# Kernel optimization log

Hardware: AMD Instinct MI355X
Metric: run time of the kernel (lower is better)

The kernel has to match this reference:

```python
import jax, jax.numpy as jnp
import numpy as np

B, T, D = 4, 1024, 1024
H, S = 16, 64            # n_heads, stalk_dim
HID = 3072               # int(D*3.0), already even
P_ADIC_BASE, P_ADIC_MAX = 2, 16


def quant6(w):
    # per-tensor symmetric 6-bit fake-quant (abs-max scale, round, clamp)
    scale = jnp.abs(w).max() / 31.0 + 1e-8
    return jnp.clip(jnp.round(w / scale), -31, 31) * scale


def q6_ste(w):
    # straight-through estimator: identity gradient
    return w + jax.lax.stop_gradient(quant6(w) - w)


def layernorm(x, g, b, eps=1e-5):
    mu = x.mean(-1, keepdims=True)
    var = ((x - mu) ** 2).mean(-1, keepdims=True)
    return (x - mu) * jax.lax.rsqrt(var + eps) * g + b


def build_p_adic_bias(t, p=P_ADIC_BASE, max_val=P_ADIC_MAX):
    idx = np.arange(t)
    d = np.abs(idx[:, None] - idx[None, :])
    nz = d > 0
    vp = np.zeros_like(d)
    work = d.copy()
    while True:
        div = nz & (work % p == 0)
        if not div.any():
            break
        vp = vp + div.astype(vp.dtype)
        work = np.where(div, work // p, work)
    vals = np.minimum(vp, max_val).astype(np.float32)
    vals = np.where(nz, vals, np.float32(max_val))
    return jnp.asarray(vals / max_val)


def setup_inputs() -> dict:
    key = jax.random.key(0)
    ks = jax.random.split(key, 12)
    sd_d = 1.0 / np.sqrt(D)
    sd_s = 1.0 / np.sqrt(S)
    sd_h = 1.0 / np.sqrt(HID)
    return {
        "x": jax.random.normal(ks[0], (B, T, D), jnp.float32),
        "wq": jax.random.normal(ks[1], (D, D), jnp.float32) * sd_d,
        "wk": jax.random.normal(ks[2], (D, D), jnp.float32) * sd_d,
        "wv": jax.random.normal(ks[3], (D, D), jnp.float32) * sd_d,
        "wo": jax.random.normal(ks[4], (D, D), jnp.float32) * sd_d,
        "su": jax.random.normal(ks[5], (S, S), jnp.float32) * sd_s,
        "sv": jax.random.normal(ks[6], (S, S), jnp.float32) * sd_s,
        "p_scale": jnp.ones((1,), jnp.float32) * 0.1,
        "norm1_g": jnp.ones((D,), jnp.float32),
        "norm1_b": jnp.zeros((D,), jnp.float32),
        "norm2_g": jnp.ones((D,), jnp.float32),
        "norm2_b": jnp.zeros((D,), jnp.float32),
        "w_up": jax.random.normal(ks[7], (HID, D), jnp.float32) * sd_d,
        "w_down": jax.random.normal(ks[8], (D, HID), jnp.float32) * sd_h,
        "theta": jnp.zeros((HID // 2,), jnp.float32),
        "mlp_norm_g": jnp.ones((HID,), jnp.float32),
        "mlp_norm_b": jnp.zeros((HID,), jnp.float32),
    }


def _sheaf_attention(xn, wq, wk, wv, wo, su, sv, p_scale):
    # projections with inline 6-bit fake-quant of weights
    Q = (xn @ q6_ste(wq).T).reshape(B, T, H, S).transpose(0, 2, 1, 3)  # [B,H,T,S]
    K = (xn @ q6_ste(wk).T).reshape(B, T, H, S).transpose(0, 2, 1, 3)
    V = (xn @ q6_ste(wv).T).reshape(B, T, H, S).transpose(0, 2, 1, 3)
    Qs = Q @ q6_ste(su).T   # stalk map on head dim
    Ks = K @ q6_ste(sv).T
    scale = 1.0 / np.sqrt(S)
    scores = jnp.einsum('bhts,bhus->bhtu', Qs, Ks) * scale
    p_bias = build_p_adic_bias(T)                     # [T,T], constant
    scores = scores + p_scale[0] * p_bias[None, None]
    causal = jnp.triu(jnp.ones((T, T), bool), k=1)
    scores = jnp.where(causal[None, None], -jnp.inf, scores)
    attn = jax.nn.softmax(scores, axis=-1)
    out = jnp.einsum('bhtu,bhus->bhts', attn, V)
    out = out.transpose(0, 2, 1, 3).reshape(B, T, D)
    return out @ q6_ste(wo).T


def _so2_mlp(xn, w_up, w_down, theta, ng, nb):
    h = xn @ q6_ste(w_up).T                          # [B,T,HID]
    hp = h.reshape(B, T, HID // 2, 2)
    a, b = hp[..., 0], hp[..., 1]
    c, s = jnp.cos(theta), jnp.sin(theta)            # [HID/2]
    rot = jnp.stack([c * a - s * b, s * a + c * b], axis=-1).reshape(B, T, HID)
    rot = layernorm(rot, ng, nb)
    rot = jax.nn.silu(rot)
    return rot @ q6_ste(w_down).T


def reference(x, wq, wk, wv, wo, su, sv, p_scale, norm1_g, norm1_b,
              norm2_g, norm2_b, w_up, w_down, theta, mlp_norm_g, mlp_norm_b):
    # pre-norm residual block: x = x + attn(ln1(x)); x = x + mlp(ln2(x))
    x = x + _sheaf_attention(layernorm(x, norm1_g, norm1_b),
                             wq, wk, wv, wo, su, sv, p_scale)
    x = x + _so2_mlp(layernorm(x, norm2_g, norm2_b),
                     w_up, w_down, theta, mlp_norm_g, mlp_norm_b)
    return x
```

## Files before the change

kernel.cpp:

```cpp
#include <hip/hip_runtime.h>
#include <stdint.h>

typedef __bf16 bf16;
typedef __attribute__((ext_vector_type(8))) __bf16 bf16x8;
typedef __attribute__((ext_vector_type(4))) __bf16 bf16x4;
typedef __attribute__((ext_vector_type(2))) __bf16 bf16x2;
typedef __attribute__((ext_vector_type(4))) float f32x4;

#define GLOBAL_AS __attribute__((address_space(1)))
#define LDS_AS __attribute__((address_space(3)))

static __device__ __forceinline__ bf16 f2bf(float f) {
  unsigned u = __builtin_bit_cast(unsigned, f);
  u += 0x7fffu + ((u >> 16) & 1u);
  unsigned short h = (unsigned short)(u >> 16);
  return __builtin_bit_cast(bf16, h);
}

static __device__ __forceinline__ float waveSum(float v) {
  #pragma unroll
  for (int o = 32; o > 0; o >>= 1) v += __shfl_xor(v, o);
  return v;
}
static __device__ __forceinline__ float waveMax(float v) {
  #pragma unroll
  for (int o = 32; o > 0; o >>= 1) v = fmaxf(v, __shfl_xor(v, o));
  return v;
}

struct QTask { const float* src; bf16* dst; int n; int slot; int blk0; };
struct QTasks { QTask t[8]; };

__global__ __launch_bounds__(256) void absmax_all(QTasks qt, unsigned* amax) {
  int ti = 0;
  #pragma unroll
  for (int i = 1; i < 8; ++i) if ((int)blockIdx.x >= qt.t[i].blk0) ti = i;
  const QTask tk = qt.t[ti];
  const int base = (blockIdx.x - tk.blk0) * 4096;
  const float4* s4 = (const float4*)(tk.src + base);
  float m = 0.f;
  #pragma unroll
  for (int i = 0; i < 4; ++i) {
    float4 w = s4[i * 256 + threadIdx.x];
    m = fmaxf(m, fmaxf(fmaxf(fabsf(w.x), fabsf(w.y)), fmaxf(fabsf(w.z), fabsf(w.w))));
  }
  m = waveMax(m);
  __shared__ float red[4];
  if ((threadIdx.x & 63) == 0) red[threadIdx.x >> 6] = m;
  __syncthreads();
  if (threadIdx.x == 0) {
    float mm = fmaxf(fmaxf(red[0], red[1]), fmaxf(red[2], red[3]));
    atomicMax(amax + tk.slot, __float_as_uint(mm));
  }
}

__global__ __launch_bounds__(256) void quant_all(QTasks qt, const unsigned* amax) {
  int ti = 0;
  #pragma unroll
  for (int i = 1; i < 8; ++i) if ((int)blockIdx.x >= qt.t[i].blk0) ti = i;
  const QTask tk = qt.t[ti];
  const float scale = __uint_as_float(amax[tk.slot]) / 31.0f + 1e-8f;
  const int base = (blockIdx.x - tk.blk0) * 4096;
  const float4* s4 = (const float4*)(tk.src + base);
  bf16x4* d4 = (bf16x4*)(tk.dst + base);
  #pragma unroll
  for (int i = 0; i < 4; ++i) {
    float4 w = s4[i * 256 + threadIdx.x];
    bf16x4 o;
    float q;
    q = fminf(31.f, fmaxf(-31.f, rintf(w.x / scale))); o[0] = f2bf(q * scale);
    q = fminf(31.f, fmaxf(-31.f, rintf(w.y / scale))); o[1] = f2bf(q * scale);
    q = fminf(31.f, fmaxf(-31.f, rintf(w.z / scale))); o[2] = f2bf(q * scale);
    q = fminf(31.f, fmaxf(-31.f, rintf(w.w / scale))); o[3] = f2bf(q * scale);
    d4[i * 256 + threadIdx.x] = o;
  }
}

__global__ __launch_bounds__(256) void ln_kernel(const float* __restrict__ x,
                                                 const float* __restrict__ g,
                                                 const float* __restrict__ b,
                                                 bf16* __restrict__ out) {
  const int row = blockIdx.x, tid = threadIdx.x;
  const float4 v = ((const float4*)(x + (size_t)row * 1024))[tid];
  float s = v.x + v.y + v.z + v.w;
  float ss = v.x * v.x + v.y * v.y + v.z * v.z + v.w * v.w;
  s = waveSum(s); ss = waveSum(ss);
  __shared__ float rs[4], rq[4];
  if ((tid & 63) == 0) { rs[tid >> 6] = s; rq[tid >> 6] = ss; }
  __syncthreads();
  s = rs[0] + rs[1] + rs[2] + rs[3];
  ss = rq[0] + rq[1] + rq[2] + rq[3];
  const float mu = s * (1.f / 1024.f);
  const float var = ss * (1.f / 1024.f) - mu * mu;
  const float rstd = rsqrtf(var + 1e-5f);
  const float4 gv = ((const float4*)g)[tid];
  const float4 bv = ((const float4*)b)[tid];
  bf16x4 o;
  o[0] = f2bf((v.x - mu) * rstd * gv.x + bv.x);
  o[1] = f2bf((v.y - mu) * rstd * gv.y + bv.y);
  o[2] = f2bf((v.z - mu) * rstd * gv.z + bv.z);
  o[3] = f2bf((v.w - mu) * rstd * gv.w + bv.w);
  ((bf16x4*)(out + (size_t)row * 1024))[tid] = o;
}

template <int OUTMODE>
__global__ __launch_bounds__(256) void gemm_bt(const bf16* __restrict__ A,
                                               const bf16* __restrict__ B,
                                               void* __restrict__ C,
                                               const float* __restrict__ Res,
                                               int M, int N, int K) {
  constexpr int BM = 128, BN = 128, BK = 32;
  __shared__ bf16 As[BM * BK];
  __shared__ bf16 Bs[BN * BK];
  const int tid = threadIdx.x;
  const int wave = tid >> 6, lane = tid & 63, quad = lane >> 4, l16 = lane & 15;
  const int bm0 = blockIdx.y * BM, bn0 = blockIdx.x * BN;
  const int wr = (wave >> 1) * 64, wc = (wave & 1) * 64;
  f32x4 acc[4][4] = {};

  for (int k0 = 0; k0 < K; k0 += BK) {
    __syncthreads();
    #pragma unroll
    for (int i = 0; i < 2; ++i) {
      const int id = tid + i * 256;
      const int r = id >> 2, c = (id & 3) * 8;
      __builtin_amdgcn_global_load_lds(
          (GLOBAL_AS void*)(A + (size_t)(bm0 + r) * K + k0 + c),
          (LDS_AS void*)(As + (size_t)(i * 256 + wave * 64) * 8), 16, 0, 0);
      __builtin_amdgcn_global_load_lds(
          (GLOBAL_AS void*)(B + (size_t)(bn0 + r) * K + k0 + c),
          (LDS_AS void*)(Bs + (size_t)(i * 256 + wave * 64) * 8), 16, 0, 0);
    }
    __syncthreads();
    bf16x8 af[4], bfr[4];
    #pragma unroll
    for (int mi = 0; mi < 4; ++mi)
      af[mi] = *(const bf16x8*)(As + (wr + mi * 16 + l16) * BK + quad * 8);
    #pragma unroll
    for (int ni = 0; ni < 4; ++ni)
      bfr[ni] = *(const bf16x8*)(Bs + (wc + ni * 16 + l16) * BK + quad * 8);
    #pragma unroll
    for (int mi = 0; mi < 4; ++mi)
      #pragma unroll
      for (int ni = 0; ni < 4; ++ni)
        acc[mi][ni] = __builtin_amdgcn_mfma_f32_16x16x32_bf16(af[mi], bfr[ni], acc[mi][ni], 0, 0, 0);
  }

  #pragma unroll
  for (int mi = 0; mi < 4; ++mi)
    #pragma unroll
    for (int ni = 0; ni < 4; ++ni)
      #pragma unroll
      for (int reg = 0; reg < 4; ++reg) {
        const int row = bm0 + wr + mi * 16 + quad * 4 + reg;
        const int col = bn0 + wc + ni * 16 + l16;
        const size_t idx = (size_t)row * N + col;
        const float v = acc[mi][ni][reg];
        if constexpr (OUTMODE == 0) ((bf16*)C)[idx] = f2bf(v);
        else if constexpr (OUTMODE == 1) ((float*)C)[idx] = v;
        else ((float*)C)[idx] = Res[idx] + v;
      }
}

__global__ __launch_bounds__(256) void stalk_kernel(const bf16* __restrict__ QKV,
                                                    const bf16* __restrict__ Su,
                                                    const bf16* __restrict__ Sv,
                                                    bf16* __restrict__ Qsout,
                                                    bf16* __restrict__ Ksout) {
  constexpr int LDP = 72;
  const int sel = blockIdx.y;
  const bf16* W = sel ? Sv : Su;
  const bf16* src = QKV + (sel ? 1024 : 0);
  bf16* out = sel ? Ksout : Qsout;
  const int vbase = blockIdx.x * 128;
  const int tid = threadIdx.x, wave = tid >> 6, lane = tid & 63, quad = lane >> 4, l16 = lane & 15;
  __shared__ bf16 Ws[64 * LDP];
  #pragma unroll
  for (int i = 0; i < 2; ++i) {
    const int cid = tid + i * 256;
    const int n = cid >> 3, c8 = (cid & 7) * 8;
    *(bf16x8*)(Ws + n * LDP + c8) = *(const bf16x8*)(W + n * 64 + c8);
  }
  __syncthreads();
  f32x4 acc[2][4] = {};
  #pragma unroll
  for (int mi = 0; mi < 2; ++mi) {
    const int v = vbase + wave * 32 + mi * 16 + l16;
    const bf16* arow = src + (size_t)(v >> 4) * 3072 + (v & 15) * 64;
    const bf16x8 a0 = *(const bf16x8*)(arow + quad * 8);
    const bf16x8 a1 = *(const bf16x8*)(arow + 32 + quad * 8);
    #pragma unroll
    for (int ni = 0; ni < 4; ++ni) {
      const bf16x8 b0 = *(const bf16x8*)(Ws + (ni * 16 + l16) * LDP + quad * 8);
      const bf16x8 b1 = *(const bf16x8*)(Ws + (ni * 16 + l16) * LDP + 32 + quad * 8);
      acc[mi][ni] = __builtin_amdgcn_mfma_f32_16x16x32_bf16(a0, b0, acc[mi][ni], 0, 0, 0);
      acc[mi][ni] = __builtin_amdgcn_mfma_f32_16x16x32_bf16(a1, b1, acc[mi][ni], 0, 0, 0);
    }
  }
  #pragma unroll
  for (int mi = 0; mi < 2; ++mi)
    #pragma unroll
    for (int ni = 0; ni < 4; ++ni)
      #pragma unroll
      for (int reg = 0; reg < 4; ++reg) {
        const int v = vbase + wave * 32 + mi * 16 + quad * 4 + reg;
        const int b = v >> 14, t = (v >> 4) & 1023, h = v & 15;
        out[(((size_t)(b * 16 + h)) * 1024 + t) * 64 + ni * 16 + l16] = f2bf(acc[mi][ni][reg]);
      }
}

__global__ __launch_bounds__(256) void v_transpose(const bf16* __restrict__ QKV,
                                                   bf16* __restrict__ Vt) {
  constexpr int LDP = 72;
  const int bh = blockIdx.x, b = bh >> 4, h = bh & 15;
  const int t0 = blockIdx.y * 64;
  const int tid = threadIdx.x;
  __shared__ bf16 tile[64 * LDP];
  #pragma unroll
  for (int i = 0; i < 2; ++i) {
    const int cid = tid + i * 256;
    const int t = cid >> 3, c8 = (cid & 7) * 8;
    *(bf16x8*)(tile + t * LDP + c8) =
        *(const bf16x8*)(QKV + ((size_t)(b * 1024 + t0 + t)) * 3072 + 2048 + h * 64 + c8);
  }
  __syncthreads();
  #pragma unroll
  for (int i = 0; i < 2; ++i) {
    const int cid = tid + i * 256;
    const int s = cid >> 3, t8 = (cid & 7) * 8;
    bf16x8 o;
    #pragma unroll
    for (int j = 0; j < 8; ++j) o[j] = tile[(t8 + j) * LDP + s];
    *(bf16x8*)(Vt + ((size_t)(bh * 64 + s)) * 1024 + t0 + t8) = o;
  }
}

__global__ __launch_bounds__(256) void attn_flash(const bf16* __restrict__ Qs,
                                                  const bf16* __restrict__ Ks,
                                                  const bf16* __restrict__ Vtg,
                                                  const float* __restrict__ p_scale_ptr,
                                                  bf16* __restrict__ out) {
  constexpr int LDP = 72;
  const int bh = blockIdx.x;
  const int b = bh >> 4, h = bh & 15;
  const int ttile = 15 - (int)blockIdx.y;
  const int t0 = ttile * 64;
  const int tid = threadIdx.x, wave = tid >> 6, lane = tid & 63, quad = lane >> 4, l16 = lane & 15;

  __shared__ bf16 Kst[64 * LDP];
  __shared__ bf16 Vt[64 * LDP];
  __shared__ bf16 Plds[4][16 * LDP];

  const float pscale2 = p_scale_ptr[0] * 1.44269504f;
  const float sc2 = 0.125f * 1.44269504f;

  const bf16* Qb = Qs + ((size_t)bh * 1024 + t0) * 64;
  const bf16* Kb = Ks + ((size_t)bh * 1024) * 64;
  const bf16* Vb = Vtg + ((size_t)bh * 64) * 1024;

  const int trow = wave * 16 + l16;
  const bf16x8 qf0 = *(const bf16x8*)(Qb + trow * 64 + quad * 8);
  const bf16x8 qf1 = *(const bf16x8*)(Qb + trow * 64 + 32 + quad * 8);

  float m[4], lsum[4];
  f32x4 Oacc[4] = {};
  #pragma unroll
  for (int r = 0; r < 4; ++r) { m[r] = -1e30f; lsum[r] = 0.f; }

  bf16x8 st[4];
  auto loadTile = [&](int u0) {
    #pragma unroll
    for (int i = 0; i < 2; ++i) {
      const int cid = tid + i * 256;
      st[i] = *(const bf16x8*)(Kb + (size_t)u0 * 64 + cid * 8);
      st[2 + i] = *(const bf16x8*)(Vb + (size_t)(cid >> 3) * 1024 + u0 + (cid & 7) * 8);
    }
  };
  loadTile(0);

  for (int ut = 0; ut <= ttile; ++ut) {
    const int u0 = ut * 64;
    #pragma unroll
    for (int i = 0; i < 2; ++i) {
      const int cid = tid + i * 256;
      const int r = cid >> 3, c8 = (cid & 7) * 8;
      *(bf16x8*)(Kst + r * LDP + c8) = st[i];
      *(bf16x8*)(Vt + r * LDP + c8) = st[2 + i];
    }
    __syncthreads();
    if (ut < ttile) loadTile(u0 + 64);

    f32x4 sc[4];
    #pragma unroll
    for (int ni = 0; ni < 4; ++ni) {
      const bf16x8 k0 = *(const bf16x8*)(Kst + (ni * 16 + l16) * LDP + quad * 8);
      const bf16x8 k1 = *(const bf16x8*)(Kst + (ni * 16 + l16) * LDP + 32 + quad * 8);
      f32x4 z = {};
      z = __builtin_amdgcn_mfma_f32_16x16x32_bf16(qf0, k0, z, 0, 0, 0);
      z = __builtin_amdgcn_mfma_f32_16x16x32_bf16(qf1, k1, z, 0, 0, 0);
      sc[ni] = z;
    }
    const bool diag = (ut == ttile);
    float pv[4][4];
    #pragma unroll
    for (int reg = 0; reg < 4; ++reg) {
      const int t = t0 + wave * 16 + quad * 4 + reg;
      float mx = -1e30f;
      #pragma unroll
      for (int ni = 0; ni < 4; ++ni) {
        const int u = u0 + ni * 16 + l16;
        const int d = t - u;
        float v = sc[ni][reg] * sc2;
        if (diag && d < 0) {
          v = -1e30f;
        } else {
          const float bias = (d == 0) ? 1.0f : (float)__builtin_ctz(d) * 0.0625f;
          v += pscale2 * bias;
        }
        pv[reg][ni] = v;
        mx = fmaxf(mx, v);
      }
      #pragma unroll
      for (int o = 1; o < 16; o <<= 1) mx = fmaxf(mx, __shfl_xor(mx, o));
      const float mnew = fmaxf(m[reg], mx);
      const float alpha = exp2f(m[reg] - mnew);
      m[reg] = mnew;
      float rs = 0.f;
      #pragma unroll
      for (int ni = 0; ni < 4; ++ni) {
        const float p = exp2f(pv[reg][ni] - mnew);
        pv[reg][ni] = p;
        rs += p;
      }
      #pragma unroll
      for (int o = 1; o < 16; o <<= 1) rs += __shfl_xor(rs, o);
      lsum[reg] = lsum[reg] * alpha + rs;
      #pragma unroll
      for (int ni = 0; ni < 4; ++ni) Oacc[ni][reg] *= alpha;
    }
    #pragma unroll
    for (int reg = 0; reg < 4; ++reg)
      #pragma unroll
      for (int ni = 0; ni < 4; ++ni)
        Plds[wave][(quad * 4 + reg) * LDP + ni * 16 + l16] = f2bf(pv[reg][ni]);
    const bf16x8 pf0 = *(const bf16x8*)(&Plds[wave][l16 * LDP + quad * 8]);
    const bf16x8 pf1 = *(const bf16x8*)(&Plds[wave][l16 * LDP + 32 + quad * 8]);
    #pragma unroll
    for (int ni = 0; ni < 4; ++ni) {
      const bf16x8 v0 = *(const bf16x8*)(Vt + (ni * 16 + l16) * LDP + quad * 8);
      const bf16x8 v1 = *(const bf16x8*)(Vt + (ni * 16 + l16) * LDP + 32 + quad * 8);
      Oacc[ni] = __builtin_amdgcn_mfma_f32_16x16x32_bf16(pf0, v0, Oacc[ni], 0, 0, 0);
      Oacc[ni] = __builtin_amdgcn_mfma_f32_16x16x32_bf16(pf1, v1, Oacc[ni], 0, 0, 0);
    }
    __syncthreads();
  }

  #pragma unroll
  for (int ni = 0; ni < 4; ++ni)
    #pragma unroll
    for (int reg = 0; reg < 4; ++reg) {
      const int t = t0 + wave * 16 + quad * 4 + reg;
      out[((size_t)(b * 1024 + t)) * 1024 + h * 64 + ni * 16 + l16] = f2bf(Oacc[ni][reg] / lsum[reg]);
    }
}

__global__ __launch_bounds__(256) void rot_ln_silu(const bf16* __restrict__ hb,
                                                   const float* __restrict__ theta,
                                                   const float* __restrict__ g,
                                                   const float* __restrict__ bb,
                                                   bf16* __restrict__ out) {
  const int row = blockIdx.x, tid = threadIdx.x;
  const bf16* hr = hb + (size_t)row * 3072;
  float r[12];
  float s = 0.f, ss = 0.f;
  #pragma unroll
  for (int i = 0; i < 6; ++i) {
    const int p = tid + i * 256;
    const bf16x2 ab = *(const bf16x2*)(hr + 2 * p);
    const float a = (float)ab[0], b_ = (float)ab[1];
    const float th = theta[p];
    const float c = cosf(th), sn = sinf(th);
    const float r0 = c * a - sn * b_;
    const float r1 = sn * a + c * b_;
    r[2 * i] = r0; r[2 * i + 1] = r1;
    s += r0 + r1;
    ss += r0 * r0 + r1 * r1;
  }
  s = waveSum(s); ss = waveSum(ss);
  __shared__ float rs_[4], rq_[4];
  if ((tid & 63) == 0) { rs_[tid >> 6] = s; rq_[tid >> 6] = ss; }
  __syncthreads();
  s = rs_[0] + rs_[1] + rs_[2] + rs_[3];
  ss = rq_[0] + rq_[1] + rq_[2] + rq_[3];
  const float mu = s * (1.f / 3072.f);
  const float var = ss * (1.f / 3072.f) - mu * mu;
  const float rstd = rsqrtf(var + 1e-5f);
  bf16* orow = out + (size_t)row * 3072;
  #pragma unroll
  for (int i = 0; i < 6; ++i) {
    const int p = tid + i * 256;
    const float2 gv = *(const float2*)(g + 2 * p);
    const float2 bv = *(const float2*)(bb + 2 * p);
    const float y0 = (r[2 * i] - mu) * rstd * gv.x + bv.x;
    const float y1 = (r[2 * i + 1] - mu) * rstd * gv.y + bv.y;
    const float o0 = y0 / (1.f + expf(-y0));
    const float o1 = y1 / (1.f + expf(-y1));
    bf16x2 o; o[0] = f2bf(o0); o[1] = f2bf(o1);
    *(bf16x2*)(orow + 2 * p) = o;
  }
}

extern "C" void kernel_launch(void* const* d_in, const int* in_sizes, int n_in,
                              void* d_out, int out_size, void* d_ws, size_t ws_size,
                              hipStream_t stream) {
  const float* x    = (const float*)d_in[0];
  const float* wq   = (const float*)d_in[1];
  const float* wk   = (const float*)d_in[2];
  const float* wv   = (const float*)d_in[3];
  const float* wo   = (const float*)d_in[4];
  const float* su   = (const float*)d_in[5];
  const float* sv   = (const float*)d_in[6];
  const float* psc  = (const float*)d_in[7];
  const float* n1g  = (const float*)d_in[8];
  const float* n1b  = (const float*)d_in[9];
  const float* n2g  = (const float*)d_in[10];
  const float* n2b  = (const float*)d_in[11];
  const float* wup  = (const float*)d_in[12];
  const float* wdn  = (const float*)d_in[13];
  const float* th   = (const float*)d_in[14];
  const float* mg   = (const float*)d_in[15];
  const float* mb   = (const float*)d_in[16];
  float* outp = (float*)d_out;

  char* ws = (char*)d_ws;
  size_t off = 0;
  auto alloc = [&](size_t bytes) { size_t o = off; off += (bytes + 255) & ~(size_t)255; return o; };
  unsigned* amax = (unsigned*)(ws + alloc(32));
  bf16* Wqkv  = (bf16*)(ws + alloc((size_t)3072 * 1024 * 2));
  bf16* Wo    = (bf16*)(ws + alloc((size_t)1024 * 1024 * 2));
  bf16* Su    = (bf16*)(ws + alloc((size_t)64 * 64 * 2));
  bf16* Sv    = (bf16*)(ws + alloc((size_t)64 * 64 * 2));
  bf16* Wup   = (bf16*)(ws + alloc((size_t)3072 * 1024 * 2));
  bf16* Wdn   = (bf16*)(ws + alloc((size_t)1024 * 3072 * 2));
  bf16* lnbuf = (bf16*)(ws + alloc((size_t)4096 * 1024 * 2));
  bf16* QKVb  = (bf16*)(ws + alloc((size_t)4096 * 3072 * 2));
  bf16* Qsb   = (bf16*)(ws + alloc((size_t)65536 * 64 * 2));
  bf16* Ksb   = (bf16*)(ws + alloc((size_t)65536 * 64 * 2));
  bf16* attno = (bf16*)(ws + alloc((size_t)4096 * 1024 * 2));
  bf16* Vtg   = (bf16*)(ws + alloc((size_t)64 * 64 * 1024 * 2));
  bf16* hbuf = QKVb;
  bf16* gbuf = Qsb;

  hipMemsetAsync(amax, 0, 32, stream);

  QTasks qt;
  int blk = 0;
  auto add = [&](int i, const float* s, bf16* d, int n) {
    qt.t[i].src = s; qt.t[i].dst = d; qt.t[i].n = n; qt.t[i].slot = i; qt.t[i].blk0 = blk;
    blk += n / 4096;
  };
  add(0, wq, Wqkv, 1024 * 1024);
  add(1, wk, Wqkv + (size_t)1024 * 1024, 1024 * 1024);
  add(2, wv, Wqkv + (size_t)2048 * 1024, 1024 * 1024);
  add(3, wo, Wo, 1024 * 1024);
  add(4, su, Su, 4096);
  add(5, sv, Sv, 4096);
  add(6, wup, Wup, 3072 * 1024);
  add(7, wdn, Wdn, 3072 * 1024);

  absmax_all<<<blk, 256, 0, stream>>>(qt, amax);
  quant_all<<<blk, 256, 0, stream>>>(qt, amax);

  ln_kernel<<<4096, 256, 0, stream>>>(x, n1g, n1b, lnbuf);
  gemm_bt<0><<<dim3(24, 32), 256, 0, stream>>>(lnbuf, Wqkv, (void*)QKVb, nullptr, 4096, 3072, 1024);
  stalk_kernel<<<dim3(512, 2), 256, 0, stream>>>(QKVb, Su, Sv, Qsb, Ksb);
  v_transpose<<<dim3(64, 16), 256, 0, stream>>>(QKVb, Vtg);
  attn_flash<<<dim3(64, 16), 256, 0, stream>>>(Qsb, Ksb, Vtg, psc, attno);
  gemm_bt<2><<<dim3(8, 32), 256, 0, stream>>>(attno, Wo, (void*)outp, x, 4096, 1024, 1024);
  ln_kernel<<<4096, 256, 0, stream>>>(outp, n2g, n2b, lnbuf);
  gemm_bt<0><<<dim3(24, 32), 256, 0, stream>>>(lnbuf, Wup, (void*)hbuf, nullptr, 4096, 3072, 1024);
  rot_ln_silu<<<4096, 256, 0, stream>>>(hbuf, th, mg, mb, gbuf);
  gemm_bt<2><<<dim3(8, 32), 256, 0, stream>>>(gbuf, Wdn, (void*)outp, outp, 4096, 1024, 3072);
}
```

Before: 417.1 us.

## Split-K the N=1024 GEMMs and fuse residual reduce with LayerNorm

```diff
diff --git a/kernel.cpp b/kernel.cpp
--- a/kernel.cpp
+++ b/kernel.cpp
@@ -103,11 +103,9 @@
   ((bf16x4*)(out + (size_t)row * 1024))[tid] = o;
 }
 
-template <int OUTMODE>
 __global__ __launch_bounds__(256) void gemm_bt(const bf16* __restrict__ A,
                                                const bf16* __restrict__ B,
-                                               void* __restrict__ C,
-                                               const float* __restrict__ Res,
+                                               bf16* __restrict__ C,
                                                int M, int N, int K) {
   constexpr int BM = 128, BN = 128, BK = 32;
   __shared__ bf16 As[BM * BK];
@@ -154,12 +152,115 @@
       for (int reg = 0; reg < 4; ++reg) {
         const int row = bm0 + wr + mi * 16 + quad * 4 + reg;
         const int col = bn0 + wc + ni * 16 + l16;
-        const size_t idx = (size_t)row * N + col;
-        const float v = acc[mi][ni][reg];
-        if constexpr (OUTMODE == 0) ((bf16*)C)[idx] = f2bf(v);
-        else if constexpr (OUTMODE == 1) ((float*)C)[idx] = v;
-        else ((float*)C)[idx] = Res[idx] + v;
+        C[(size_t)row * N + col] = f2bf(acc[mi][ni][reg]);
       }
+}
+
+__global__ __launch_bounds__(256) void gemm_bt_split(const bf16* __restrict__ A,
+                                                     const bf16* __restrict__ B,
+                                                     float* __restrict__ P,
+                                                     int M, int N, int Kfull, int Kper) {
+  constexpr int BM = 128, BN = 128, BK = 32;
+  __shared__ bf16 As[BM * BK];
+  __shared__ bf16 Bs[BN * BK];
+  const int tid = threadIdx.x;
+  const int wave = tid >> 6, lane = tid & 63, quad = lane >> 4, l16 = lane & 15;
+  const int bm0 = blockIdx.y * BM, bn0 = blockIdx.x * BN;
+  const int wr = (wave >> 1) * 64, wc = (wave & 1) * 64;
+  const int kbeg = blockIdx.z * Kper, kend = kbeg + Kper;
+  float* Pz = P + (size_t)blockIdx.z * M * N;
+  f32x4 acc[4][4] = {};
+
+  for (int k0 = kbeg; k0 < kend; k0 += BK) {
+    __syncthreads();
+    #pragma unroll
+    for (int i = 0; i < 2; ++i) {
+      const int id = tid + i * 256;
+      const int r = id >> 2, c = (id & 3) * 8;
+      __builtin_amdgcn_global_load_lds(
+          (GLOBAL_AS void*)(A + (size_t)(bm0 + r) * Kfull + k0 + c),
+          (LDS_AS void*)(As + (size_t)(i * 256 + wave * 64) * 8), 16, 0, 0);
+      __builtin_amdgcn_global_load_lds(
+          (GLOBAL_AS void*)(B + (size_t)(bn0 + r) * Kfull + k0 + c),
+          (LDS_AS void*)(Bs + (size_t)(i * 256 + wave * 64) * 8), 16, 0, 0);
+    }
+    __syncthreads();
+    bf16x8 af[4], bfr[4];
+    #pragma unroll
+    for (int mi = 0; mi < 4; ++mi)
+      af[mi] = *(const bf16x8*)(As + (wr + mi * 16 + l16) * BK + quad * 8);
+    #pragma unroll
+    for (int ni = 0; ni < 4; ++ni)
+      bfr[ni] = *(const bf16x8*)(Bs + (wc + ni * 16 + l16) * BK + quad * 8);
+    #pragma unroll
+    for (int mi = 0; mi < 4; ++mi)
+      #pragma unroll
+      for (int ni = 0; ni < 4; ++ni)
+        acc[mi][ni] = __builtin_amdgcn_mfma_f32_16x16x32_bf16(af[mi], bfr[ni], acc[mi][ni], 0, 0, 0);
+  }
+
+  #pragma unroll
+  for (int mi = 0; mi < 4; ++mi)
+    #pragma unroll
+    for (int ni = 0; ni < 4; ++ni)
+      #pragma unroll
+      for (int reg = 0; reg < 4; ++reg) {
+        const int row = bm0 + wr + mi * 16 + quad * 4 + reg;
+        const int col = bn0 + wc + ni * 16 + l16;
+        Pz[(size_t)row * N + col] = acc[mi][ni][reg];
+      }
+}
+
+__global__ __launch_bounds__(256) void reduce_wo_ln(const float* __restrict__ x,
+                                                    const float* __restrict__ P,
+                                                    const float* __restrict__ g,
+                                                    const float* __restrict__ b,
+                                                    float* __restrict__ y,
+                                                    bf16* __restrict__ lnout) {
+  const int row = blockIdx.x, tid = threadIdx.x;
+  const size_t base = (size_t)row * 1024;
+  const float4 vx = ((const float4*)(x + base))[tid];
+  const float4 p0 = ((const float4*)(P + base))[tid];
+  const float4 p1 = ((const float4*)(P + base + (size_t)4096 * 1024))[tid];
+  float4 v;
+  v.x = vx.x + p0.x + p1.x;
+  v.y = vx.y + p0.y + p1.y;
+  v.z = vx.z + p0.z + p1.z;
+  v.w = vx.w + p0.w + p1.w;
+  ((float4*)(y + base))[tid] = v;
+  float s = v.x + v.y + v.z + v.w;
+  float ss = v.x * v.x + v.y * v.y + v.z * v.z + v.w * v.w;
+  s = waveSum(s); ss = waveSum(ss);
+  __shared__ float rs[4], rq[4];
+  if ((tid & 63) == 0) { rs[tid >> 6] = s; rq[tid >> 6] = ss; }
+  __syncthreads();
+  s = rs[0] + rs[1] + rs[2] + rs[3];
+  ss = rq[0] + rq[1] + rq[2] + rq[3];
+  const float mu = s * (1.f / 1024.f);
+  const float var = ss * (1.f / 1024.f) - mu * mu;
+  const float rstd = rsqrtf(var + 1e-5f);
+  const float4 gv = ((const float4*)g)[tid];
+  const float4 bv = ((const float4*)b)[tid];
+  bf16x4 o;
+  o[0] = f2bf((v.x - mu) * rstd * gv.x + bv.x);
+  o[1] = f2bf((v.y - mu) * rstd * gv.y + bv.y);
+  o[2] = f2bf((v.z - mu) * rstd * gv.z + bv.z);
+  o[3] = f2bf((v.w - mu) * rstd * gv.w + bv.w);
+  ((bf16x4*)(lnout + base))[tid] = o;
+}
+
+__global__ __launch_bounds__(256) void reduce_down(float* __restrict__ y,
+                                                   const float* __restrict__ P) {
+  const size_t i = (size_t)blockIdx.x * 256 + threadIdx.x;
+  const float4 vy = ((const float4*)y)[i];
+  const float4 p0 = ((const float4*)P)[i];
+  const float4 p1 = ((const float4*)(P + (size_t)4096 * 1024))[i];
+  float4 v;
+  v.x = vy.x + p0.x + p1.x;
+  v.y = vy.y + p0.y + p1.y;
+  v.z = vy.z + p0.z + p1.z;
+  v.w = vy.w + p0.w + p1.w;
+  ((float4*)y)[i] = v;
 }
 
 __global__ __launch_bounds__(256) void stalk_kernel(const bf16* __restrict__ QKV,
@@ -446,8 +547,9 @@
   bf16* QKVb  = (bf16*)(ws + alloc((size_t)4096 * 3072 * 2));
   bf16* Qsb   = (bf16*)(ws + alloc((size_t)65536 * 64 * 2));
   bf16* Ksb   = (bf16*)(ws + alloc((size_t)65536 * 64 * 2));
+  bf16* Vtg   = (bf16*)(ws + alloc((size_t)64 * 64 * 1024 * 2));
   bf16* attno = (bf16*)(ws + alloc((size_t)4096 * 1024 * 2));
-  bf16* Vtg   = (bf16*)(ws + alloc((size_t)64 * 64 * 1024 * 2));
+  float* Pbuf = (float*)(ws + alloc((size_t)2 * 4096 * 1024 * 4));
   bf16* hbuf = QKVb;
   bf16* gbuf = Qsb;
 
@@ -472,13 +574,14 @@
   quant_all<<<blk, 256, 0, stream>>>(qt, amax);
 
   ln_kernel<<<4096, 256, 0, stream>>>(x, n1g, n1b, lnbuf);
-  gemm_bt<0><<<dim3(24, 32), 256, 0, stream>>>(lnbuf, Wqkv, (void*)QKVb, nullptr, 4096, 3072, 1024);
+  gemm_bt<<<dim3(24, 32), 256, 0, stream>>>(lnbuf, Wqkv, QKVb, 4096, 3072, 1024);
   stalk_kernel<<<dim3(512, 2), 256, 0, stream>>>(QKVb, Su, Sv, Qsb, Ksb);
   v_transpose<<<dim3(64, 16), 256, 0, stream>>>(QKVb, Vtg);
   attn_flash<<<dim3(64, 16), 256, 0, stream>>>(Qsb, Ksb, Vtg, psc, attno);
-  gemm_bt<2><<<dim3(8, 32), 256, 0, stream>>>(attno, Wo, (void*)outp, x, 4096, 1024, 1024);
-  ln_kernel<<<4096, 256, 0, stream>>>(outp, n2g, n2b, lnbuf);
-  gemm_bt<0><<<dim3(24, 32), 256, 0, stream>>>(lnbuf, Wup, (void*)hbuf, nullptr, 4096, 3072, 1024);
+  gemm_bt_split<<<dim3(8, 32, 2), 256, 0, stream>>>(attno, Wo, Pbuf, 4096, 1024, 1024, 512);
+  reduce_wo_ln<<<4096, 256, 0, stream>>>(x, Pbuf, n2g, n2b, outp, lnbuf);
+  gemm_bt<<<dim3(24, 32), 256, 0, stream>>>(lnbuf, Wup, hbuf, 4096, 3072, 1024);
   rot_ln_silu<<<4096, 256, 0, stream>>>(hbuf, th, mg, mb, gbuf);
-  gemm_bt<2><<<dim3(8, 32), 256, 0, stream>>>(gbuf, Wdn, (void*)outp, outp, 4096, 1024, 3072);
-}
+  gemm_bt_split<<<dim3(8, 32, 2), 256, 0, stream>>>(gbuf, Wdn, Pbuf, 4096, 1024, 3072, 1536);
+  reduce_down<<<4096, 256, 0, stream>>>(outp, Pbuf);
+}
```

Measured after the change: 399.8 us. -4.1%, faster.
